# Kernel optimization log

Hardware: AMD Instinct MI355X
Metric: run time of the kernel (lower is better)

## Reference

```python
import jax, jax.numpy as jnp
import numpy as np

B, T, N, C, H = 64, 12, 1370, 8, 64

def setup_inputs() -> dict:
    key = jax.random.key(0)
    ks = jax.random.split(key, 7)
    s_ih = 1.0 / np.sqrt(H)
    inp = {
        "x": jax.random.normal(ks[0], (B, T, N, C), dtype=jnp.float32),
        # PyTorch nn.LSTM params, gate order (i, f, g, o)
        "W_ih": jax.random.uniform(ks[1], (4 * H, C), jnp.float32, -s_ih, s_ih),
        "W_hh": jax.random.uniform(ks[2], (4 * H, H), jnp.float32, -s_ih, s_ih),
        "b_ih": jax.random.uniform(ks[3], (4 * H,), jnp.float32, -s_ih, s_ih),
        "b_hh": jax.random.uniform(ks[4], (4 * H,), jnp.float32, -s_ih, s_ih),
        "W_fc": jax.random.uniform(ks[5], (C, H), jnp.float32, -s_ih, s_ih),
        "b_fc": jax.random.uniform(ks[6], (C,), jnp.float32, -s_ih, s_ih),
    }
    return inp

def reference(x, W_ih, W_hh, b_ih, b_hh, W_fc, b_fc):
    Bx, Tx, Nx, Cx = x.shape
    Hh = W_hh.shape[1]
    # (B, T, N, C) -> (B*N, T, C): shared-weight LSTM over all node sequences
    xr = jnp.transpose(x, (0, 2, 1, 3)).reshape(Bx * Nx, Tx, Cx)
    # Precompute input projections for all timesteps: (B*N, T, 4H)
    x_gates = jnp.einsum('btc,gc->btg', xr, W_ih) + b_ih
    # time-major for scan: (T, B*N, 4H)
    x_gates = jnp.moveaxis(x_gates, 1, 0)

    def step(carry, xg):
        h, c = carry
        gates = xg + h @ W_hh.T + b_hh  # (B*N, 4H)
        i, f, g, o = jnp.split(gates, 4, axis=-1)
        i = jax.nn.sigmoid(i)
        f = jax.nn.sigmoid(f)
        g = jnp.tanh(g)
        o = jax.nn.sigmoid(o)
        c = f * c + i * g
        h = o * jnp.tanh(c)
        return (h, c), None

    h0 = jnp.zeros((Bx * Nx, Hh), dtype=x.dtype)
    c0 = jnp.zeros((Bx * Nx, Hh), dtype=x.dtype)
    (h_last, _), _ = jax.lax.scan(step, (h0, c0), x_gates)

    y_flat = h_last @ W_fc.T + b_fc  # (B*N, C)
    return y_flat.reshape(Bx, Nx, Cx)
```

## Files before the change

kernel.cpp:

```cpp
#include <hip/hip_runtime.h>

#define T_ 12
#define N_ 1370
#define MSEQ 64
#define NT 4
#define LDA 72
#define NBLK 1370

typedef __attribute__((ext_vector_type(8))) short short8;
typedef __attribute__((ext_vector_type(4))) float floatx4;
typedef __attribute__((ext_vector_type(4))) unsigned uint4v;
typedef __attribute__((ext_vector_type(2))) unsigned uint2v;

#define NLOG2E -1.4426950408889634f
#define TLOG2E 2.8853900817779268f
#define N2LOG2E -5.7707801635558536f

__device__ __forceinline__ short f2bf(float x) {
  unsigned u = __builtin_bit_cast(unsigned, x);
  u = (u + 0x7fffu + ((u >> 16) & 1u)) >> 16;
  return (short)u;
}
__device__ __forceinline__ unsigned pk_bf16(float a, float b) {
  unsigned r;
  asm("v_cvt_pk_bf16_f32 %0, %1, %2" : "=v"(r) : "v"(a), "v"(b));
  return r;
}
__device__ __forceinline__ short8 load_w8s(const float* __restrict__ p, float s) {
  floatx4 a = *(const floatx4*)p;
  floatx4 b = *(const floatx4*)(p + 4);
  uint4v u = {pk_bf16(a[0] * s, a[1] * s), pk_bf16(a[2] * s, a[3] * s),
              pk_bf16(b[0] * s, b[1] * s), pk_bf16(b[2] * s, b[3] * s)};
  return __builtin_bit_cast(short8, u);
}

__global__ void __launch_bounds__(256, 4) lstm_kernel(
    const float* __restrict__ x, const float* __restrict__ W_ih,
    const float* __restrict__ W_hh, const float* __restrict__ b_ih,
    const float* __restrict__ b_hh, const float* __restrict__ W_fc,
    const float* __restrict__ b_fc, float* __restrict__ out) {
  __shared__ short hbuf[2][MSEQ][LDA];
  __shared__ __align__(16) short xbuf[T_][MSEQ][8];
  __shared__ __align__(16) short ones_row[8];

  const int tid = threadIdx.x;
  const int wave = tid >> 6;
  const int lane = tid & 63;
  const int m16 = lane & 15;
  const int q = lane >> 4;
  const int blk = blockIdx.x;

  const int urow = wave * 16 + m16;
  short8 wA[4][3];
#pragma unroll
  for (int g = 0; g < 4; ++g) {
    const float sg = (g == 2) ? TLOG2E : NLOG2E;
    const int grow = g * 64 + urow;
    const float* wr = W_hh + grow * 64;
    wA[g][0] = load_w8s(wr + q * 8, sg);
    wA[g][1] = load_w8s(wr + 32 + q * 8, sg);
    short8 z = {0, 0, 0, 0, 0, 0, 0, 0};
    if (q == 0) {
      wA[g][2] = load_w8s(W_ih + grow * 8, sg);
    } else if (q == 1) {
      z[0] = f2bf(sg * (b_ih[grow] + b_hh[grow]));
      wA[g][2] = z;
    } else {
      wA[g][2] = z;
    }
  }

  {
    int* hp = (int*)hbuf;
#pragma unroll
    for (int i = tid; i < (2 * MSEQ * LDA) / 2; i += 256) hp[i] = 0;
    if (tid < 8) ones_row[tid] = (tid == 0) ? (short)0x3F80 : (short)0;
  }

  {
#pragma unroll
    for (int j = 0; j < 6; ++j) {
      const int slot = j * 256 + tid;
      const int t = slot >> 7;
      const int idx = slot & 127;
      const int seq = idx >> 1;
      const int half = idx & 1;
      const int s0 = blk * MSEQ + seq;
      const int bidx = s0 / N_;
      const int nidx = s0 - bidx * N_;
      const floatx4 v = *(const floatx4*)(
          x + (((size_t)bidx * T_ + t) * N_ + nidx) * 8 + half * 4);
      uint2v u = {pk_bf16(v[0], v[1]), pk_bf16(v[2], v[3])};
      *(uint2v*)&xbuf[t][seq][half * 4] = u;
    }
  }
  __syncthreads();

  const floatx4 zacc = {0.0f, 0.0f, 0.0f, 0.0f};

  float cst[NT][4];
#pragma unroll
  for (int nt = 0; nt < NT; ++nt)
#pragma unroll
    for (int r = 0; r < 4; ++r) cst[nt][r] = 0.0f;

  for (int t = 0; t < T_; ++t) {
    const int rb = t & 1, wb = rb ^ 1;
#pragma unroll
    for (int nt = 0; nt < NT; ++nt) {
      const int srow = nt * 16 + m16;
      short8 b0 = *(const short8*)&hbuf[rb][srow][q * 8];
      short8 b1 = *(const short8*)&hbuf[rb][srow][32 + q * 8];
      const short* bxp = q ? &ones_row[0] : &xbuf[t][srow][0];
      short8 bx = *(const short8*)bxp;
      floatx4 gi = __builtin_amdgcn_mfma_f32_16x16x32_bf16(wA[0][0], b0, zacc, 0, 0, 0);
      floatx4 gf = __builtin_amdgcn_mfma_f32_16x16x32_bf16(wA[1][0], b0, zacc, 0, 0, 0);
      floatx4 gg = __builtin_amdgcn_mfma_f32_16x16x32_bf16(wA[2][0], b0, zacc, 0, 0, 0);
      floatx4 go = __builtin_amdgcn_mfma_f32_16x16x32_bf16(wA[3][0], b0, zacc, 0, 0, 0);
      gi = __builtin_amdgcn_mfma_f32_16x16x32_bf16(wA[0][1], b1, gi, 0, 0, 0);
      gf = __builtin_amdgcn_mfma_f32_16x16x32_bf16(wA[1][1], b1, gf, 0, 0, 0);
      gg = __builtin_amdgcn_mfma_f32_16x16x32_bf16(wA[2][1], b1, gg, 0, 0, 0);
      go = __builtin_amdgcn_mfma_f32_16x16x32_bf16(wA[3][1], b1, go, 0, 0, 0);
      gi = __builtin_amdgcn_mfma_f32_16x16x32_bf16(wA[0][2], bx, gi, 0, 0, 0);
      gf = __builtin_amdgcn_mfma_f32_16x16x32_bf16(wA[1][2], bx, gf, 0, 0, 0);
      gg = __builtin_amdgcn_mfma_f32_16x16x32_bf16(wA[2][2], bx, gg, 0, 0, 0);
      go = __builtin_amdgcn_mfma_f32_16x16x32_bf16(wA[3][2], bx, go, 0, 0, 0);
      float hv[4];
#pragma unroll
      for (int r = 0; r < 4; ++r) {
        float di = 1.0f + __builtin_amdgcn_exp2f(gi[r]);
        float df = 1.0f + __builtin_amdgcn_exp2f(gf[r]);
        float dg = 1.0f + __builtin_amdgcn_exp2f(gg[r]);
        float dq = 1.0f + __builtin_amdgcn_exp2f(go[r]);
        float pa = di * df, pb = dg * dq;
        float rp = __builtin_amdgcn_rcpf(pa * pb);
        float fv = rp * di * pb;
        float rpa = rp * pa;
        float ov = rpa * dg;
        float tg = fmaf(TLOG2E, dg, N2LOG2E);
        float ig = tg * rp * (df * dq);
        float cs = fmaf(fv, cst[nt][r], ig);
        cst[nt][r] = cs;
        float dt = 1.0f + __builtin_amdgcn_exp2f(cs);
        float tc = fmaf(-2.0f, __builtin_amdgcn_rcpf(dt), 1.0f);
        hv[r] = ov * tc;
      }
      unsigned long long pk =
          (unsigned long long)pk_bf16(hv[0], hv[1]) |
          ((unsigned long long)pk_bf16(hv[2], hv[3]) << 32);
      *(unsigned long long*)&hbuf[wb][srow][wave * 16 + q * 4] = pk;
    }
    __syncthreads();
  }

  {
    short8 f0, f1;
    short8 z = {0, 0, 0, 0, 0, 0, 0, 0};
    if (m16 < 8) {
      const float* wr = W_fc + m16 * 64;
      f0 = load_w8s(wr + q * 8, 1.0f);
      f1 = load_w8s(wr + 32 + q * 8, 1.0f);
    } else {
      f0 = z;
      f1 = z;
    }
    const int srow = wave * 16 + m16;
    short8 h0 = *(const short8*)&hbuf[0][srow][q * 8];
    short8 h1 = *(const short8*)&hbuf[0][srow][32 + q * 8];
    floatx4 acc = __builtin_amdgcn_mfma_f32_16x16x32_bf16(f0, h0, zacc, 0, 0, 0);
    acc = __builtin_amdgcn_mfma_f32_16x16x32_bf16(f1, h1, acc, 0, 0, 0);
    if (q < 2) {
      const int orow = blk * MSEQ + srow;
#pragma unroll
      for (int r = 0; r < 4; ++r)
        out[orow * 8 + q * 4 + r] = acc[r] + b_fc[q * 4 + r];
    }
  }
}

extern "C" void kernel_launch(void* const* d_in, const int* in_sizes, int n_in,
                              void* d_out, int out_size, void* d_ws,
                              size_t ws_size, hipStream_t stream) {
  const float* x    = (const float*)d_in[0];
  const float* W_ih = (const float*)d_in[1];
  const float* W_hh = (const float*)d_in[2];
  const float* b_ih = (const float*)d_in[3];
  const float* b_hh = (const float*)d_in[4];
  const float* W_fc = (const float*)d_in[5];
  const float* b_fc = (const float*)d_in[6];
  float* out = (float*)d_out;
  hipLaunchKernelGGL(lstm_kernel, dim3(NBLK), dim3(256), 0, stream,
                     x, W_ih, W_hh, b_ih, b_hh, W_fc, b_fc, out);
}
```

Baseline: 170.6 us.

## Repartition LSTM work so each wave owns sequences, removing per-step block barriers

Each wave now handles 16 sequences across all 64 hidden units instead of 16 hidden units across all 64 sequences. Its recurrent state then stays in a private per-wave LDS strip, so the __syncthreads at every timestep goes away. The full W_hh is held in registers as 32 fragments, and the input-projection and bias fragments are staged in LDS and reloaded each step. The cost is much higher register pressure: launch bounds drop to 2 blocks per SM, which lowers occupancy and adds LDS reads for the W_ih fragments.

```diff
diff --git a/kernel.cpp b/kernel.cpp
--- a/kernel.cpp
+++ b/kernel.cpp
@@ -3,9 +3,9 @@
 #define T_ 12
 #define N_ 1370
 #define MSEQ 64
-#define NT 4
 #define LDA 72
 #define NBLK 1370
+#define NFRAG 48
 
 typedef __attribute__((ext_vector_type(8))) short short8;
 typedef __attribute__((ext_vector_type(4))) float floatx4;
@@ -34,12 +34,13 @@
   return __builtin_bit_cast(short8, u);
 }
 
-__global__ void __launch_bounds__(256, 4) lstm_kernel(
+__global__ void __launch_bounds__(256, 2) lstm_kernel(
     const float* __restrict__ x, const float* __restrict__ W_ih,
     const float* __restrict__ W_hh, const float* __restrict__ b_ih,
     const float* __restrict__ b_hh, const float* __restrict__ W_fc,
     const float* __restrict__ b_fc, float* __restrict__ out) {
-  __shared__ short hbuf[2][MSEQ][LDA];
+  __shared__ short wlds[NFRAG][64][8];
+  __shared__ short hstrip[4][2][16][LDA];
   __shared__ __align__(16) short xbuf[T_][MSEQ][8];
   __shared__ __align__(16) short ones_row[8];
 
@@ -50,30 +51,34 @@
   const int q = lane >> 4;
   const int blk = blockIdx.x;
 
-  const int urow = wave * 16 + m16;
-  short8 wA[4][3];
-#pragma unroll
-  for (int g = 0; g < 4; ++g) {
-    const float sg = (g == 2) ? TLOG2E : NLOG2E;
-    const int grow = g * 64 + urow;
-    const float* wr = W_hh + grow * 64;
-    wA[g][0] = load_w8s(wr + q * 8, sg);
-    wA[g][1] = load_w8s(wr + 32 + q * 8, sg);
-    short8 z = {0, 0, 0, 0, 0, 0, 0, 0};
-    if (q == 0) {
-      wA[g][2] = load_w8s(W_ih + grow * 8, sg);
-    } else if (q == 1) {
-      z[0] = f2bf(sg * (b_ih[grow] + b_hh[grow]));
-      wA[g][2] = z;
+#pragma unroll
+  for (int i = 0; i < 12; ++i) {
+    const int fid = wave * 12 + i;
+    short8 v = {0, 0, 0, 0, 0, 0, 0, 0};
+    if (fid < 32) {
+      const int gu = fid >> 1, kc = fid & 1;
+      const int g = gu >> 2, ut = gu & 3;
+      const float sg = (g == 2) ? TLOG2E : NLOG2E;
+      const int grow = g * 64 + ut * 16 + m16;
+      v = load_w8s(W_hh + grow * 64 + kc * 32 + q * 8, sg);
     } else {
-      wA[g][2] = z;
-    }
+      const int gu = fid - 32;
+      const int g = gu >> 2, ut = gu & 3;
+      const float sg = (g == 2) ? TLOG2E : NLOG2E;
+      const int grow = g * 64 + ut * 16 + m16;
+      if (q == 0) {
+        v = load_w8s(W_ih + grow * 8, sg);
+      } else if (q == 1) {
+        v[0] = f2bf(sg * (b_ih[grow] + b_hh[grow]));
+      }
+    }
+    *(short8*)&wlds[fid][lane][0] = v;
   }
 
   {
-    int* hp = (int*)hbuf;
-#pragma unroll
-    for (int i = tid; i < (2 * MSEQ * LDA) / 2; i += 256) hp[i] = 0;
+    int* hp = (int*)hstrip;
+#pragma unroll
+    for (int i = tid; i < (int)(sizeof(hstrip) / 4); i += 256) hp[i] = 0;
     if (tid < 8) ones_row[tid] = (tid == 0) ? (short)0x3F80 : (short)0;
   }
 
@@ -96,35 +101,49 @@
   }
   __syncthreads();
 
+  short8 wA[4][4][2];
+#pragma unroll
+  for (int g = 0; g < 4; ++g)
+#pragma unroll
+    for (int ut = 0; ut < 4; ++ut)
+#pragma unroll
+      for (int kc = 0; kc < 2; ++kc)
+        wA[g][ut][kc] =
+            *(const short8*)&wlds[(((g << 2) | ut) << 1) | kc][lane][0];
+
   const floatx4 zacc = {0.0f, 0.0f, 0.0f, 0.0f};
 
-  float cst[NT][4];
-#pragma unroll
-  for (int nt = 0; nt < NT; ++nt)
-#pragma unroll
-    for (int r = 0; r < 4; ++r) cst[nt][r] = 0.0f;
-
+  float cst[4][4];
+#pragma unroll
+  for (int ut = 0; ut < 4; ++ut)
+#pragma unroll
+    for (int r = 0; r < 4; ++r) cst[ut][r] = 0.0f;
+
+#pragma unroll 2
   for (int t = 0; t < T_; ++t) {
     const int rb = t & 1, wb = rb ^ 1;
-#pragma unroll
-    for (int nt = 0; nt < NT; ++nt) {
-      const int srow = nt * 16 + m16;
-      short8 b0 = *(const short8*)&hbuf[rb][srow][q * 8];
-      short8 b1 = *(const short8*)&hbuf[rb][srow][32 + q * 8];
-      const short* bxp = q ? &ones_row[0] : &xbuf[t][srow][0];
-      short8 bx = *(const short8*)bxp;
-      floatx4 gi = __builtin_amdgcn_mfma_f32_16x16x32_bf16(wA[0][0], b0, zacc, 0, 0, 0);
-      floatx4 gf = __builtin_amdgcn_mfma_f32_16x16x32_bf16(wA[1][0], b0, zacc, 0, 0, 0);
-      floatx4 gg = __builtin_amdgcn_mfma_f32_16x16x32_bf16(wA[2][0], b0, zacc, 0, 0, 0);
-      floatx4 go = __builtin_amdgcn_mfma_f32_16x16x32_bf16(wA[3][0], b0, zacc, 0, 0, 0);
-      gi = __builtin_amdgcn_mfma_f32_16x16x32_bf16(wA[0][1], b1, gi, 0, 0, 0);
-      gf = __builtin_amdgcn_mfma_f32_16x16x32_bf16(wA[1][1], b1, gf, 0, 0, 0);
-      gg = __builtin_amdgcn_mfma_f32_16x16x32_bf16(wA[2][1], b1, gg, 0, 0, 0);
-      go = __builtin_amdgcn_mfma_f32_16x16x32_bf16(wA[3][1], b1, go, 0, 0, 0);
-      gi = __builtin_amdgcn_mfma_f32_16x16x32_bf16(wA[0][2], bx, gi, 0, 0, 0);
-      gf = __builtin_amdgcn_mfma_f32_16x16x32_bf16(wA[1][2], bx, gf, 0, 0, 0);
-      gg = __builtin_amdgcn_mfma_f32_16x16x32_bf16(wA[2][2], bx, gg, 0, 0, 0);
-      go = __builtin_amdgcn_mfma_f32_16x16x32_bf16(wA[3][2], bx, go, 0, 0, 0);
+    short8 b0 = *(const short8*)&hstrip[wave][rb][m16][q * 8];
+    short8 b1 = *(const short8*)&hstrip[wave][rb][m16][32 + q * 8];
+    const short* bxp = q ? &ones_row[0] : &xbuf[t][wave * 16 + m16][0];
+    short8 bx = *(const short8*)bxp;
+#pragma unroll
+    for (int ut = 0; ut < 4; ++ut) {
+      short8 wx0 = *(const short8*)&wlds[32 + ut][lane][0];
+      short8 wx1 = *(const short8*)&wlds[36 + ut][lane][0];
+      short8 wx2 = *(const short8*)&wlds[40 + ut][lane][0];
+      short8 wx3 = *(const short8*)&wlds[44 + ut][lane][0];
+      floatx4 gi = __builtin_amdgcn_mfma_f32_16x16x32_bf16(wA[0][ut][0], b0, zacc, 0, 0, 0);
+      floatx4 gf = __builtin_amdgcn_mfma_f32_16x16x32_bf16(wA[1][ut][0], b0, zacc, 0, 0, 0);
+      floatx4 gg = __builtin_amdgcn_mfma_f32_16x16x32_bf16(wA[2][ut][0], b0, zacc, 0, 0, 0);
+      floatx4 go = __builtin_amdgcn_mfma_f32_16x16x32_bf16(wA[3][ut][0], b0, zacc, 0, 0, 0);
+      gi = __builtin_amdgcn_mfma_f32_16x16x32_bf16(wA[0][ut][1], b1, gi, 0, 0, 0);
+      gf = __builtin_amdgcn_mfma_f32_16x16x32_bf16(wA[1][ut][1], b1, gf, 0, 0, 0);
+      gg = __builtin_amdgcn_mfma_f32_16x16x32_bf16(wA[2][ut][1], b1, gg, 0, 0, 0);
+      go = __builtin_amdgcn_mfma_f32_16x16x32_bf16(wA[3][ut][1], b1, go, 0, 0, 0);
+      gi = __builtin_amdgcn_mfma_f32_16x16x32_bf16(wx0, bx, gi, 0, 0, 0);
+      gf = __builtin_amdgcn_mfma_f32_16x16x32_bf16(wx1, bx, gf, 0, 0, 0);
+      gg = __builtin_amdgcn_mfma_f32_16x16x32_bf16(wx2, bx, gg, 0, 0, 0);
+      go = __builtin_amdgcn_mfma_f32_16x16x32_bf16(wx3, bx, go, 0, 0, 0);
       float hv[4];
 #pragma unroll
       for (int r = 0; r < 4; ++r) {
@@ -139,8 +158,8 @@
         float ov = rpa * dg;
         float tg = fmaf(TLOG2E, dg, N2LOG2E);
         float ig = tg * rp * (df * dq);
-        float cs = fmaf(fv, cst[nt][r], ig);
-        cst[nt][r] = cs;
+        float cs = fmaf(fv, cst[ut][r], ig);
+        cst[ut][r] = cs;
         float dt = 1.0f + __builtin_amdgcn_exp2f(cs);
         float tc = fmaf(-2.0f, __builtin_amdgcn_rcpf(dt), 1.0f);
         hv[r] = ov * tc;
@@ -148,9 +167,8 @@
       unsigned long long pk =
           (unsigned long long)pk_bf16(hv[0], hv[1]) |
           ((unsigned long long)pk_bf16(hv[2], hv[3]) << 32);
-      *(unsigned long long*)&hbuf[wb][srow][wave * 16 + q * 4] = pk;
-    }
-    __syncthreads();
+      *(unsigned long long*)&hstrip[wave][wb][m16][ut * 16 + q * 4] = pk;
+    }
   }
 
   {
@@ -164,13 +182,12 @@
       f0 = z;
       f1 = z;
     }
-    const int srow = wave * 16 + m16;
-    short8 h0 = *(const short8*)&hbuf[0][srow][q * 8];
-    short8 h1 = *(const short8*)&hbuf[0][srow][32 + q * 8];
+    short8 h0 = *(const short8*)&hstrip[wave][0][m16][q * 8];
+    short8 h1 = *(const short8*)&hstrip[wave][0][m16][32 + q * 8];
     floatx4 acc = __builtin_amdgcn_mfma_f32_16x16x32_bf16(f0, h0, zacc, 0, 0, 0);
     acc = __builtin_amdgcn_mfma_f32_16x16x32_bf16(f1, h1, acc, 0, 0, 0);
     if (q < 2) {
-      const int orow = blk * MSEQ + srow;
+      const int orow = blk * MSEQ + wave * 16 + m16;
 #pragma unroll
       for (int r = 0; r < 4; ++r)
         out[orow * 8 + q * 4 + r] = acc[r] + b_fc[q * 4 + r];
```

New measurement: 172.5 us. No clear change (+1.1%).
